# Kernel tuning notes

Hardware: AMD Instinct MI355X
Metric: run time of the kernel (lower is better)

## Reference

```python
import jax, jax.numpy as jnp
import numpy as np

EPS = 1e-8  # torch CosineSimilarity default eps


def setup_inputs() -> dict:
    key = jax.random.key(0)
    k1, k2, k3 = jax.random.split(key, 3)
    B, H, Lq, Lc, D = 8, 16, 128, 4096, 1024
    return {
        "question_emb": jax.random.normal(k1, (B, Lq, D), dtype=jnp.float32),
        "context_emb": jax.random.normal(k2, (B, Lc, D), dtype=jnp.float32),
        "cross_attn_weights": jax.random.uniform(k3, (B, H, Lq, Lc), dtype=jnp.float32),
    }


def reference(question_emb, context_emb, cross_attn_weights, topk: int = 5):
    # avg attention over heads and query tokens -> [B, Lc]
    avg_attn = cross_attn_weights.mean(axis=(1, 2))
    k = min(topk, context_emb.shape[1])
    _, idx = jax.lax.top_k(avg_attn, k)  # idx: [B, k]
    # gather top-k context vectors: [B, k, D]
    top_ctx = jnp.take_along_axis(context_emb, idx[:, :, None], axis=1)
    # mean question vector per batch: [B, D]
    q_vec = question_emb.mean(axis=1)
    # cosine similarity with torch-style eps clamping on each norm
    q_norm = jnp.maximum(jnp.linalg.norm(q_vec, axis=-1, keepdims=True), EPS)  # [B,1]
    c_norm = jnp.maximum(jnp.linalg.norm(top_ctx, axis=-1), EPS)               # [B,k]
    dots = jnp.einsum("bd,bkd->bk", q_vec, top_ctx)
    sim = dots / (q_norm * c_norm)  # [B, k]
    # per-batch mean of (1 - sim), then mean over batch (k is constant -> global mean)
    return (1.0 - sim).mean()
```

## Files before the change

kernel.cpp:

```cpp
#include <hip/hip_runtime.h>
#include <math.h>

#define BB 8
#define HH 16
#define LQ 128
#define LC 4096
#define DD 1024
#define ROWS (HH * LQ)
#define R_SLABS 32
#define ROWS_PER_SLAB (ROWS / R_SLABS)
#define COL_TILES 4
#define KTOP 5
#define EPSF 1e-8f

__global__ __launch_bounds__(256) void k1_col_partials(
    const float* __restrict__ attn, float* __restrict__ partials,
    float* __restrict__ out) {
    if (blockIdx.x == 0 && threadIdx.x == 0) *out = 0.0f;

    int blk = blockIdx.x;
    int r = blk % R_SLABS;
    int t = blk / R_SLABS;
    int ct = t % COL_TILES;
    int b = t / COL_TILES;
    int col = ct * 1024 + threadIdx.x * 4;

    const float4* src = (const float4*)(attn + (size_t)b * ROWS * LC
                                             + (size_t)r * ROWS_PER_SLAB * LC + col);
    float4 acc = make_float4(0.f, 0.f, 0.f, 0.f);
#pragma unroll 8
    for (int m = 0; m < ROWS_PER_SLAB; ++m) {
        float4 v = src[(size_t)m * (LC / 4)];
        acc.x += v.x; acc.y += v.y; acc.z += v.z; acc.w += v.w;
    }
    float4* dst = (float4*)(partials + (size_t)r * BB * LC + (size_t)b * LC + col);
    *dst = acc;
}

__global__ __launch_bounds__(256) void k23_reduce(
    const float* __restrict__ partials, const float* __restrict__ q,
    float* __restrict__ avg, float* __restrict__ qv) {
    int blk = blockIdx.x;
    if (blk < (BB * LC) / 256) {
        int g = blk * 256 + threadIdx.x;
        float s = 0.f;
#pragma unroll
        for (int r = 0; r < R_SLABS; ++r)
            s += partials[(size_t)r * BB * LC + g];
        avg[g] = s;
    } else {
        int g = (blk - (BB * LC) / 256) * 256 + threadIdx.x;
        int b = g / DD;
        int d = g % DD;
        const float* p = q + (size_t)b * LQ * DD + d;
        float s = 0.f;
#pragma unroll 8
        for (int row = 0; row < LQ; ++row)
            s += p[(size_t)row * DD];
        qv[g] = s * (1.0f / LQ);
    }
}

__global__ __launch_bounds__(256) void k4_finalize(
    const float* __restrict__ avg, const float* __restrict__ qv,
    const float* __restrict__ ctx, float* __restrict__ out) {
    __shared__ float swv[4];
    __shared__ int   swi[4];
    __shared__ int   s_win;
    __shared__ int   s_top[KTOP];
    __shared__ float sred[4][11];

    int b = blockIdx.x;
    int tid = threadIdx.x;
    int lane = tid & 63;
    int wave = tid >> 6;

    float v[16];
#pragma unroll
    for (int j = 0; j < 16; ++j)
        v[j] = avg[(size_t)b * LC + j * 256 + tid];

    for (int kk = 0; kk < KTOP; ++kk) {
        float bv = v[0];
        int bj = 0;
#pragma unroll
        for (int j = 1; j < 16; ++j)
            if (v[j] > bv) { bv = v[j]; bj = j; }
        int bc = bj * 256 + tid;

        for (int off = 32; off > 0; off >>= 1) {
            float ov = __shfl_down(bv, off);
            int   oc = __shfl_down(bc, off);
            if (ov > bv || (ov == bv && oc < bc)) { bv = ov; bc = oc; }
        }
        if (lane == 0) { swv[wave] = bv; swi[wave] = bc; }
        __syncthreads();
        if (tid == 0) {
            float fv = swv[0]; int fc = swi[0];
#pragma unroll
            for (int w = 1; w < 4; ++w)
                if (swv[w] > fv || (swv[w] == fv && swi[w] < fc)) { fv = swv[w]; fc = swi[w]; }
            s_top[kk] = fc;
            s_win = fc;
        }
        __syncthreads();
        int wc = s_win;
        if ((wc & 255) == tid) v[wc >> 8] = -3.0e38f;
    }

    const float4 q4 = *((const float4*)(qv + (size_t)b * DD + tid * 4));
    float acc[11];
    acc[10] = q4.x * q4.x + q4.y * q4.y + q4.z * q4.z + q4.w * q4.w;
#pragma unroll
    for (int kk = 0; kk < KTOP; ++kk) {
        const float4 c4 = *((const float4*)(ctx + (size_t)b * LC * DD
                                            + (size_t)s_top[kk] * DD + tid * 4));
        acc[kk]        = q4.x * c4.x + q4.y * c4.y + q4.z * c4.z + q4.w * c4.w;
        acc[5 + kk]    = c4.x * c4.x + c4.y * c4.y + c4.z * c4.z + c4.w * c4.w;
    }
    for (int off = 32; off > 0; off >>= 1) {
#pragma unroll
        for (int i = 0; i < 11; ++i)
            acc[i] += __shfl_down(acc[i], off);
    }
    if (lane == 0) {
#pragma unroll
        for (int i = 0; i < 11; ++i) sred[wave][i] = acc[i];
    }
    __syncthreads();
    if (tid == 0) {
        float t[11];
#pragma unroll
        for (int i = 0; i < 11; ++i)
            t[i] = sred[0][i] + sred[1][i] + sred[2][i] + sred[3][i];
        float qn = fmaxf(sqrtf(t[10]), EPSF);
        float loss = 0.f;
#pragma unroll
        for (int kk = 0; kk < KTOP; ++kk) {
            float cn = fmaxf(sqrtf(t[5 + kk]), EPSF);
            loss += 1.0f - t[kk] / (qn * cn);
        }
        atomicAdd(out, loss * (1.0f / (BB * KTOP)));
    }
}

extern "C" void kernel_launch(void* const* d_in, const int* in_sizes, int n_in,
                              void* d_out, int out_size, void* d_ws, size_t ws_size,
                              hipStream_t stream) {
    const float* q    = (const float*)d_in[0];
    const float* ctx  = (const float*)d_in[1];
    const float* attn = (const float*)d_in[2];
    float* out = (float*)d_out;

    float* partials = (float*)d_ws;
    float* avg = partials + (size_t)R_SLABS * BB * LC;
    float* qv  = avg + (size_t)BB * LC;

    k1_col_partials<<<BB * COL_TILES * R_SLABS, 256, 0, stream>>>(attn, partials, out);
    k23_reduce<<<(BB * LC) / 256 + (BB * DD) / 256, 256, 0, stream>>>(partials, q, avg, qv);
    k4_finalize<<<BB, 256, 0, stream>>>(avg, qv, ctx, out);
}
```

Before: 423.4 us.

## Fuse slab reduction into top-k kernel and move question mean into first kernel

```diff
diff --git a/kernel.cpp b/kernel.cpp
--- a/kernel.cpp
+++ b/kernel.cpp
@@ -10,46 +10,37 @@
 #define R_SLABS 32
 #define ROWS_PER_SLAB (ROWS / R_SLABS)
 #define COL_TILES 4
+#define K1_BLOCKS (BB * COL_TILES * R_SLABS)
+#define QV_BLOCKS ((BB * DD) / 256)
 #define KTOP 5
 #define EPSF 1e-8f
 
-__global__ __launch_bounds__(256) void k1_col_partials(
-    const float* __restrict__ attn, float* __restrict__ partials,
+__global__ __launch_bounds__(256) void kA_partials_qv(
+    const float* __restrict__ attn, const float* __restrict__ q,
+    float* __restrict__ partials, float* __restrict__ qv,
     float* __restrict__ out) {
     if (blockIdx.x == 0 && threadIdx.x == 0) *out = 0.0f;
 
     int blk = blockIdx.x;
-    int r = blk % R_SLABS;
-    int t = blk / R_SLABS;
-    int ct = t % COL_TILES;
-    int b = t / COL_TILES;
-    int col = ct * 1024 + threadIdx.x * 4;
+    if (blk < K1_BLOCKS) {
+        int r = blk % R_SLABS;
+        int t = blk / R_SLABS;
+        int ct = t % COL_TILES;
+        int b = t / COL_TILES;
+        int col = ct * 1024 + threadIdx.x * 4;
 
-    const float4* src = (const float4*)(attn + (size_t)b * ROWS * LC
-                                             + (size_t)r * ROWS_PER_SLAB * LC + col);
-    float4 acc = make_float4(0.f, 0.f, 0.f, 0.f);
+        const float4* src = (const float4*)(attn + (size_t)b * ROWS * LC
+                                                 + (size_t)r * ROWS_PER_SLAB * LC + col);
+        float4 acc = make_float4(0.f, 0.f, 0.f, 0.f);
 #pragma unroll 8
-    for (int m = 0; m < ROWS_PER_SLAB; ++m) {
-        float4 v = src[(size_t)m * (LC / 4)];
-        acc.x += v.x; acc.y += v.y; acc.z += v.z; acc.w += v.w;
-    }
-    float4* dst = (float4*)(partials + (size_t)r * BB * LC + (size_t)b * LC + col);
-    *dst = acc;
-}
-
-__global__ __launch_bounds__(256) void k23_reduce(
-    const float* __restrict__ partials, const float* __restrict__ q,
-    float* __restrict__ avg, float* __restrict__ qv) {
-    int blk = blockIdx.x;
-    if (blk < (BB * LC) / 256) {
-        int g = blk * 256 + threadIdx.x;
-        float s = 0.f;
-#pragma unroll
-        for (int r = 0; r < R_SLABS; ++r)
-            s += partials[(size_t)r * BB * LC + g];
-        avg[g] = s;
+        for (int m = 0; m < ROWS_PER_SLAB; ++m) {
+            float4 v = src[(size_t)m * (LC / 4)];
+            acc.x += v.x; acc.y += v.y; acc.z += v.z; acc.w += v.w;
+        }
+        float4* dst = (float4*)(partials + (size_t)r * BB * LC + (size_t)b * LC + col);
+        *dst = acc;
     } else {
-        int g = (blk - (BB * LC) / 256) * 256 + threadIdx.x;
+        int g = (blk - K1_BLOCKS) * 256 + threadIdx.x;
         int b = g / DD;
         int d = g % DD;
         const float* p = q + (size_t)b * LQ * DD + d;
@@ -61,11 +52,11 @@
     }
 }
 
-__global__ __launch_bounds__(256) void k4_finalize(
-    const float* __restrict__ avg, const float* __restrict__ qv,
+__global__ __launch_bounds__(1024) void kB_topk_finalize(
+    const float* __restrict__ partials, const float* __restrict__ qv,
     const float* __restrict__ ctx, float* __restrict__ out) {
-    __shared__ float swv[4];
-    __shared__ int   swi[4];
+    __shared__ float swv[16];
+    __shared__ int   swi[16];
     __shared__ int   s_win;
     __shared__ int   s_top[KTOP];
     __shared__ float sred[4][11];
@@ -75,18 +66,21 @@
     int lane = tid & 63;
     int wave = tid >> 6;
 
-    float v[16];
+    float v[4] = {0.f, 0.f, 0.f, 0.f};
+    const float* pb = partials + (size_t)b * LC + (size_t)tid * 4;
 #pragma unroll
-    for (int j = 0; j < 16; ++j)
-        v[j] = avg[(size_t)b * LC + j * 256 + tid];
+    for (int r = 0; r < R_SLABS; ++r) {
+        float4 p = *(const float4*)(pb + (size_t)r * BB * LC);
+        v[0] += p.x; v[1] += p.y; v[2] += p.z; v[3] += p.w;
+    }
 
     for (int kk = 0; kk < KTOP; ++kk) {
         float bv = v[0];
         int bj = 0;
 #pragma unroll
-        for (int j = 1; j < 16; ++j)
+        for (int j = 1; j < 4; ++j)
             if (v[j] > bv) { bv = v[j]; bj = j; }
-        int bc = bj * 256 + tid;
+        int bc = tid * 4 + bj;
 
         for (int off = 32; off > 0; off >>= 1) {
             float ov = __shfl_down(bv, off);
@@ -98,34 +92,36 @@
         if (tid == 0) {
             float fv = swv[0]; int fc = swi[0];
 #pragma unroll
-            for (int w = 1; w < 4; ++w)
+            for (int w = 1; w < 16; ++w)
                 if (swv[w] > fv || (swv[w] == fv && swi[w] < fc)) { fv = swv[w]; fc = swi[w]; }
             s_top[kk] = fc;
             s_win = fc;
         }
         __syncthreads();
         int wc = s_win;
-        if ((wc & 255) == tid) v[wc >> 8] = -3.0e38f;
+        if ((wc >> 2) == tid) v[wc & 3] = -3.0e38f;
     }
 
-    const float4 q4 = *((const float4*)(qv + (size_t)b * DD + tid * 4));
-    float acc[11];
-    acc[10] = q4.x * q4.x + q4.y * q4.y + q4.z * q4.z + q4.w * q4.w;
+    if (tid < 256) {
+        const float4 q4 = *((const float4*)(qv + (size_t)b * DD + tid * 4));
+        float acc[11];
+        acc[10] = q4.x * q4.x + q4.y * q4.y + q4.z * q4.z + q4.w * q4.w;
 #pragma unroll
-    for (int kk = 0; kk < KTOP; ++kk) {
-        const float4 c4 = *((const float4*)(ctx + (size_t)b * LC * DD
-                                            + (size_t)s_top[kk] * DD + tid * 4));
-        acc[kk]        = q4.x * c4.x + q4.y * c4.y + q4.z * c4.z + q4.w * c4.w;
-        acc[5 + kk]    = c4.x * c4.x + c4.y * c4.y + c4.z * c4.z + c4.w * c4.w;
-    }
-    for (int off = 32; off > 0; off >>= 1) {
+        for (int kk = 0; kk < KTOP; ++kk) {
+            const float4 c4 = *((const float4*)(ctx + (size_t)b * LC * DD
+                                                + (size_t)s_top[kk] * DD + tid * 4));
+            acc[kk]     = q4.x * c4.x + q4.y * c4.y + q4.z * c4.z + q4.w * c4.w;
+            acc[5 + kk] = c4.x * c4.x + c4.y * c4.y + c4.z * c4.z + c4.w * c4.w;
+        }
+        for (int off = 32; off > 0; off >>= 1) {
 #pragma unroll
-        for (int i = 0; i < 11; ++i)
-            acc[i] += __shfl_down(acc[i], off);
-    }
-    if (lane == 0) {
+            for (int i = 0; i < 11; ++i)
+                acc[i] += __shfl_down(acc[i], off);
+        }
+        if (lane == 0) {
 #pragma unroll
-        for (int i = 0; i < 11; ++i) sred[wave][i] = acc[i];
+            for (int i = 0; i < 11; ++i) sred[wave][i] = acc[i];
+        }
     }
     __syncthreads();
     if (tid == 0) {
@@ -153,10 +149,8 @@
     float* out = (float*)d_out;
 
     float* partials = (float*)d_ws;
-    float* avg = partials + (size_t)R_SLABS * BB * LC;
-    float* qv  = avg + (size_t)BB * LC;
+    float* qv = partials + (size_t)R_SLABS * BB * LC;
 
-    k1_col_partials<<<BB * COL_TILES * R_SLABS, 256, 0, stream>>>(attn, partials, out);
-    k23_reduce<<<(BB * LC) / 256 + (BB * DD) / 256, 256, 0, stream>>>(partials, q, avg, qv);
-    k4_finalize<<<BB, 256, 0, stream>>>(avg, qv, ctx, out);
+    kA_partials_qv<<<K1_BLOCKS + QV_BLOCKS, 256, 0, stream>>>(attn, q, partials, qv, out);
+    kB_topk_finalize<<<BB, 1024, 0, stream>>>(partials, qv, ctx, out);
 }
```

New measurement: 427.1 us. About the same (+0.9%).
